# Performance work log

Measured on AMD Instinct MI355X. Metric: run time of the kernel, lower is better.

Reference implementation:

```python
import jax, jax.numpy as jnp
import numpy as np

S, B, I, H, L = 512, 64, 512, 512, 2
EPS = 1e-5


def setup_inputs() -> dict:
    key = jax.random.key(0)
    ks = jax.random.split(key, 8)
    gain = float(np.sqrt(1.0 / H))
    u = lambda k, shp: jax.random.uniform(k, shp, jnp.float32, -gain, gain)
    return {
        "inputs": jax.random.normal(ks[0], (S, B, I), jnp.float32),
        "h0": jnp.zeros((L, B, H), jnp.float32),
        "c0": jnp.zeros((L, B, H), jnp.float32),
        "wx0": u(ks[1], (I, 4 * H)),
        "wx1": u(ks[2], (H, 4 * H)),
        "wh0": u(ks[3], (H, 4 * H)),
        "wh1": u(ks[4], (H, 4 * H)),
        "bias": u(ks[5], (L, 4 * H)),
        "ln_gamma": jnp.ones((L, 4, H), jnp.float32),
        "ln_beta": jnp.zeros((L, 4, H), jnp.float32),
    }


def _layer(x, h, c, wx, wh, b, gamma, beta):
    # Precompute the input projection as one big GEMM: [S,B,4H]
    xg = jnp.einsum('sbi,ig->sbg', x, wx) + b

    def cell(carry, xg_t):
        h, c = carry
        gate = xg_t + h @ wh                      # [B, 4H]
        g = gate.reshape(B, 4, H)
        mu = jnp.mean(g, axis=-1, keepdims=True)
        var = jnp.var(g, axis=-1, keepdims=True)
        g = (g - mu) * jax.lax.rsqrt(var + EPS) * gamma + beta
        i, f, o, u = g[:, 0], g[:, 1], g[:, 2], g[:, 3]
        c = jax.nn.sigmoid(f) * c + jax.nn.sigmoid(i) * jnp.tanh(u)
        h = jax.nn.sigmoid(o) * jnp.tanh(c)
        return (h, c), h

    (h, c), ys = jax.lax.scan(cell, (h, c), xg)
    return ys, h, c


def reference(inputs, h0, c0, wx0, wx1, wh0, wh1, bias, ln_gamma, ln_beta):
    x = inputs
    wxs, whs = [wx0, wx1], [wh0, wh1]
    hs, cs = [], []
    for l in range(L):
        x, h, c = _layer(x, h0[l], c0[l], wxs[l], whs[l], bias[l], ln_gamma[l], ln_beta[l])
        hs.append(h)
        cs.append(c)
    return x, jnp.stack(hs, 0), jnp.stack(cs, 0)
```

## Files before the change

kernel.cpp:

```cpp
#include <hip/hip_runtime.h>


typedef float f32x4 __attribute__((ext_vector_type(4)));

__device__ __forceinline__ float sigm(float x) { return 1.f / (1.f + __expf(-x)); }
__device__ __forceinline__ float tanh_f(float x) { return 2.f / (1.f + __expf(-2.f * x)) - 1.f; }

__global__ void init_k(const float* __restrict__ h0, const float* __restrict__ c0,
                       float* __restrict__ h_T, float* __restrict__ c_ws) {
  const int nthr = gridDim.x * 256;
  for (int i = blockIdx.x * 256 + threadIdx.x; i < 2 * 64 * 512; i += nthr) {
    int l = i >> 15, rem = i & 32767, b = rem >> 9, hc = rem & 511;
    h_T[(l * 512 + hc) * 64 + b] = h0[i];
    c_ws[i] = c0[i];
  }
}

__global__ __launch_bounds__(256)
void gemm_step(const float* __restrict__ inputs,
               const float* __restrict__ wx0, const float* __restrict__ wx1,
               const float* __restrict__ wh0, const float* __restrict__ wh1,
               const float* __restrict__ bias,
               const float* __restrict__ h_T, const float* __restrict__ y0_T,
               float* __restrict__ gates_ws, int tau)
{
  extern __shared__ float lds[];
  float* W_lds = lds;
  float* A_lds = lds + 16384;
  float* part  = lds + 33792;

  const int tid = threadIdx.x;
  const int wg = blockIdx.x;
  const int layer = wg >> 7;
  const int w = wg & 127;
  if (layer == 0 ? (tau >= 512) : (tau < 1)) return;
  const int t = layer ? (tau - 1) : tau;

  const int wavet = tid >> 6, lane = tid & 63;
  const int rq = lane & 15;
  const int gq = lane >> 4;
  const int srow = tid >> 2, sg = tid & 3;

  const float* Wx = layer ? wx1 : wx0;
  const float* Wh = layer ? wh1 : wh0;

  for (int i = 0; i < 16; ++i) {
    int e = tid + i * 256;
    int k = e >> 2, g = e & 3;
    const float* src = (k < 512) ? (Wx + (size_t)k * 2048)
                                 : (Wh + (size_t)(k - 512) * 2048);
    *(f32x4*)&W_lds[k * 16 + g * 4] = *(const f32x4*)(src + g * 512 + 4 * w);
  }
  __syncthreads();

  f32x4 biasr = *(const f32x4*)(bias + layer * 2048 + sg * 512 + 4 * w);
  f32x4 acc[4];
#pragma unroll
  for (int r = 0; r < 4; ++r) acc[r] = (f32x4){0.f, 0.f, 0.f, 0.f};

  {
    const float* hT = h_T + layer * 32768;
    const int k0 = wavet * 128;
#pragma unroll 8
    for (int kk = 0; kk < 128; ++kk) {
      int k = k0 + kk;
      f32x4 av = *(const f32x4*)&hT[k * 64 + 4 * rq];
      f32x4 wv = *(const f32x4*)&W_lds[(512 + k) * 16 + gq * 4];
      acc[0] += av[0] * wv;
      acc[1] += av[1] * wv;
      acc[2] += av[2] * wv;
      acc[3] += av[3] * wv;
    }
  }

  if (layer == 1) {
    const int k0 = wavet * 128;
#pragma unroll 8
    for (int kk = 0; kk < 128; ++kk) {
      int k = k0 + kk;
      f32x4 av = *(const f32x4*)&y0_T[k * 64 + 4 * rq];
      f32x4 wv = *(const f32x4*)&W_lds[k * 16 + gq * 4];
      acc[0] += av[0] * wv;
      acc[1] += av[1] * wv;
      acc[2] += av[2] * wv;
      acc[3] += av[3] * wv;
    }
  } else {
    const float* xsrc = inputs + (size_t)t * 32768;
    const int strow = rq + 16 * wavet;
    f32x4 st[8];
    auto LOADC = [&](int koff) {
      const float* s = xsrc + strow * 512 + koff;
#pragma unroll
      for (int i = 0; i < 8; ++i)
        st[i] = *(const f32x4*)(s + 4 * (gq + 4 * i));
    };
    auto WRITEC = [&](int b) {
      float* dst = A_lds + b * 8704;
#pragma unroll
      for (int i = 0; i < 8; ++i) {
        int kq = gq + 4 * i;
#pragma unroll
        for (int j = 0; j < 4; ++j)
          dst[(4 * kq + j) * 68 + strow] = st[i][j];
      }
    };
    LOADC(0);
    WRITEC(0);
    __syncthreads();
#pragma unroll 1
    for (int i = 0; i < 4; ++i) {
      if (i < 3) LOADC((i + 1) * 128);
      const float* Ab = A_lds + (i & 1) * 8704;
      const int kg = i * 128 + wavet * 32;
#pragma unroll 8
      for (int kk = 0; kk < 32; ++kk) {
        int k = wavet * 32 + kk;
        f32x4 av = *(const f32x4*)&Ab[k * 68 + 4 * rq];
        f32x4 wv = *(const f32x4*)&W_lds[(kg + kk) * 16 + gq * 4];
        acc[0] += av[0] * wv;
        acc[1] += av[1] * wv;
        acc[2] += av[2] * wv;
        acc[3] += av[3] * wv;
      }
      if (i < 3) WRITEC((i + 1) & 1);
      __syncthreads();
    }
  }

#pragma unroll
  for (int r = 0; r < 4; ++r)
#pragma unroll
    for (int cc = 0; cc < 4; ++cc)
      part[(wavet * 64 + 4 * rq + r) * 17 + gq * 4 + cc] = acc[r][cc];
  __syncthreads();
  {
    f32x4 pre;
#pragma unroll
    for (int cc = 0; cc < 4; ++cc) {
      float v = biasr[cc];
      v += part[(0 * 64 + srow) * 17 + sg * 4 + cc];
      v += part[(1 * 64 + srow) * 17 + sg * 4 + cc];
      v += part[(2 * 64 + srow) * 17 + sg * 4 + cc];
      v += part[(3 * 64 + srow) * 17 + sg * 4 + cc];
      pre[cc] = v;
    }
    *(f32x4*)&gates_ws[((size_t)layer * 64 + srow) * 2048 + sg * 512 + 4 * w] = pre;
  }
}

__global__ __launch_bounds__(256)
void cell_step(const float* __restrict__ gates_ws,
               const float* __restrict__ gamma_, const float* __restrict__ beta_,
               float* __restrict__ c_ws, float* __restrict__ h_T,
               float* __restrict__ y0_T, float* __restrict__ out, int tau)
{
  __shared__ float sred[512];
  __shared__ float minv[8];
  __shared__ float gnorm[2048];

  const int tid = threadIdx.x;
  const int wgid = blockIdx.x;
  const int l = wgid >> 6, b = wgid & 63;
  if (l == 0 ? (tau >= 512) : (tau < 1)) return;
  const int t = l ? (tau - 1) : tau;

  const float* grow = gates_ws + ((size_t)l * 64 + b) * 2048;
  const int c0i = tid * 8;
  float acc[8];
#pragma unroll
  for (int j = 0; j < 8; ++j) acc[j] = grow[c0i + j];

  {
    float s = 0.f, ss = 0.f;
#pragma unroll
    for (int j = 0; j < 8; ++j) { s += acc[j]; ss += acc[j] * acc[j]; }
    sred[tid * 2] = s; sred[tid * 2 + 1] = ss;
  }
  __syncthreads();
  if (tid < 4) {
    float S = 0.f, SS = 0.f;
    for (int u = 0; u < 64; ++u) {
      S += sred[(tid * 64 + u) * 2];
      SS += sred[(tid * 64 + u) * 2 + 1];
    }
    float mu = S * (1.f / 512.f);
    float var = SS * (1.f / 512.f) - mu * mu;
    minv[tid * 2] = mu;
    minv[tid * 2 + 1] = rsqrtf(fmaxf(var, 0.f) + 1e-5f);
  }
  __syncthreads();
  {
    int g = tid >> 6;
    float mu = minv[g * 2], inv = minv[g * 2 + 1];
#pragma unroll
    for (int j = 0; j < 8; ++j) {
      int c = c0i + j;
      gnorm[c] = (acc[j] - mu) * inv * gamma_[l * 2048 + c] + beta_[l * 2048 + c];
    }
  }
  __syncthreads();

#pragma unroll
  for (int v = 0; v < 2; ++v) {
    int hc = tid * 2 + v;
    float ig = sigm(gnorm[hc]);
    float fg = sigm(gnorm[512 + hc]);
    float og = sigm(gnorm[1024 + hc]);
    float ug = tanh_f(gnorm[1536 + hc]);
    float cs = fg * c_ws[l * 32768 + b * 512 + hc] + ig * ug;
    float hv = og * tanh_f(cs);
    c_ws[l * 32768 + b * 512 + hc] = cs;
    h_T[(l * 512 + hc) * 64 + b] = hv;
    if (l == 0) y0_T[hc * 64 + b] = hv;
    else        out[(size_t)t * 32768 + b * 512 + hc] = hv;
    if (t == 511) {
      out[16777216 + l * 32768 + b * 512 + hc] = hv;
      out[16842752 + l * 32768 + b * 512 + hc] = cs;
    }
  }
}

extern "C" void kernel_launch(void* const* d_in, const int* in_sizes, int n_in,
                              void* d_out, int out_size, void* d_ws, size_t ws_size,
                              hipStream_t stream) {
  const float* inputs = (const float*)d_in[0];
  const float* h0 = (const float*)d_in[1];
  const float* c0 = (const float*)d_in[2];
  const float* wx0 = (const float*)d_in[3];
  const float* wx1 = (const float*)d_in[4];
  const float* wh0 = (const float*)d_in[5];
  const float* wh1 = (const float*)d_in[6];
  const float* bias = (const float*)d_in[7];
  const float* gamma_ = (const float*)d_in[8];
  const float* beta_ = (const float*)d_in[9];
  float* out = (float*)d_out;

  char* ws = (char*)d_ws;
  float* gates_ws = (float*)ws;
  float* h_T = (float*)(ws + 1048576);
  float* y0_T = (float*)(ws + 1310720);
  float* c_ws = (float*)(ws + 1441792);

  const int smem_bytes = 38144 * 4;
  hipFuncSetAttribute((const void*)gemm_step,
                      hipFuncAttributeMaxDynamicSharedMemorySize, smem_bytes);

  hipLaunchKernelGGL(init_k, dim3(256), dim3(256), 0, stream, h0, c0, h_T, c_ws);

  for (int tau = 0; tau <= 512; ++tau) {
    hipLaunchKernelGGL(gemm_step, dim3(256), dim3(256), smem_bytes, stream,
                       inputs, wx0, wx1, wh0, wh1, bias, h_T, y0_T, gates_ws, tau);
    hipLaunchKernelGGL(cell_step, dim3(128), dim3(256), 0, stream,
                       gates_ws, gamma_, beta_, c_ws, h_T, y0_T, out, tau);
  }
}
```

Baseline: 20.71 ms.

## Pre-transpose next timestep's input in cell kernel, drop LDS transpose in GEMM

Layer-0 GEMM blocks no longer load the input slice and transpose it through LDS with double buffering. Instead, the cell_step kernel transposes the next timestep's input into a ping-pong x_T buffer, and init_k transposes step 0. The GEMM then reads x_T directly from global memory, the same way it reads h_T. This removes the per-block redundant transpose, several barriers and about 68KB of LDS, which may allow more blocks per CU. The cost is uncoalesced strided reads in cell_step and a new cross-kernel dependency on the ping-pong buffer.

```diff
diff --git a/kernel.cpp b/kernel.cpp
--- a/kernel.cpp
+++ b/kernel.cpp
@@ -6,18 +6,24 @@
 __device__ __forceinline__ float sigm(float x) { return 1.f / (1.f + __expf(-x)); }
 __device__ __forceinline__ float tanh_f(float x) { return 2.f / (1.f + __expf(-2.f * x)) - 1.f; }
 
-__global__ void init_k(const float* __restrict__ h0, const float* __restrict__ c0,
-                       float* __restrict__ h_T, float* __restrict__ c_ws) {
+__global__ void init_k(const float* __restrict__ inputs,
+                       const float* __restrict__ h0, const float* __restrict__ c0,
+                       float* __restrict__ h_T, float* __restrict__ c_ws,
+                       float* __restrict__ x_T) {
   const int nthr = gridDim.x * 256;
   for (int i = blockIdx.x * 256 + threadIdx.x; i < 2 * 64 * 512; i += nthr) {
     int l = i >> 15, rem = i & 32767, b = rem >> 9, hc = rem & 511;
     h_T[(l * 512 + hc) * 64 + b] = h0[i];
     c_ws[i] = c0[i];
   }
+  for (int i = blockIdx.x * 256 + threadIdx.x; i < 512 * 64; i += nthr) {
+    int k = i >> 6, b = i & 63;
+    x_T[k * 64 + b] = inputs[b * 512 + k];
+  }
 }
 
 __global__ __launch_bounds__(256)
-void gemm_step(const float* __restrict__ inputs,
+void gemm_step(const float* __restrict__ x_T,
                const float* __restrict__ wx0, const float* __restrict__ wx1,
                const float* __restrict__ wh0, const float* __restrict__ wh1,
                const float* __restrict__ bias,
@@ -26,15 +32,13 @@
 {
   extern __shared__ float lds[];
   float* W_lds = lds;
-  float* A_lds = lds + 16384;
-  float* part  = lds + 33792;
+  float* part  = lds + 16384;
 
   const int tid = threadIdx.x;
   const int wg = blockIdx.x;
   const int layer = wg >> 7;
   const int w = wg & 127;
   if (layer == 0 ? (tau >= 512) : (tau < 1)) return;
-  const int t = layer ? (tau - 1) : tau;
 
   const int wavet = tid >> 6, lane = tid & 63;
   const int rq = lane & 15;
@@ -58,75 +62,22 @@
 #pragma unroll
   for (int r = 0; r < 4; ++r) acc[r] = (f32x4){0.f, 0.f, 0.f, 0.f};
 
-  {
-    const float* hT = h_T + layer * 32768;
+  auto GEMMT = [&](const float* T, int wbase) {
     const int k0 = wavet * 128;
 #pragma unroll 8
     for (int kk = 0; kk < 128; ++kk) {
       int k = k0 + kk;
-      f32x4 av = *(const f32x4*)&hT[k * 64 + 4 * rq];
-      f32x4 wv = *(const f32x4*)&W_lds[(512 + k) * 16 + gq * 4];
+      f32x4 av = *(const f32x4*)&T[k * 64 + 4 * rq];
+      f32x4 wv = *(const f32x4*)&W_lds[(wbase + k) * 16 + gq * 4];
       acc[0] += av[0] * wv;
       acc[1] += av[1] * wv;
       acc[2] += av[2] * wv;
       acc[3] += av[3] * wv;
     }
-  }
-
-  if (layer == 1) {
-    const int k0 = wavet * 128;
-#pragma unroll 8
-    for (int kk = 0; kk < 128; ++kk) {
-      int k = k0 + kk;
-      f32x4 av = *(const f32x4*)&y0_T[k * 64 + 4 * rq];
-      f32x4 wv = *(const f32x4*)&W_lds[k * 16 + gq * 4];
-      acc[0] += av[0] * wv;
-      acc[1] += av[1] * wv;
-      acc[2] += av[2] * wv;
-      acc[3] += av[3] * wv;
-    }
-  } else {
-    const float* xsrc = inputs + (size_t)t * 32768;
-    const int strow = rq + 16 * wavet;
-    f32x4 st[8];
-    auto LOADC = [&](int koff) {
-      const float* s = xsrc + strow * 512 + koff;
-#pragma unroll
-      for (int i = 0; i < 8; ++i)
-        st[i] = *(const f32x4*)(s + 4 * (gq + 4 * i));
-    };
-    auto WRITEC = [&](int b) {
-      float* dst = A_lds + b * 8704;
-#pragma unroll
-      for (int i = 0; i < 8; ++i) {
-        int kq = gq + 4 * i;
-#pragma unroll
-        for (int j = 0; j < 4; ++j)
-          dst[(4 * kq + j) * 68 + strow] = st[i][j];
-      }
-    };
-    LOADC(0);
-    WRITEC(0);
-    __syncthreads();
-#pragma unroll 1
-    for (int i = 0; i < 4; ++i) {
-      if (i < 3) LOADC((i + 1) * 128);
-      const float* Ab = A_lds + (i & 1) * 8704;
-      const int kg = i * 128 + wavet * 32;
-#pragma unroll 8
-      for (int kk = 0; kk < 32; ++kk) {
-        int k = wavet * 32 + kk;
-        f32x4 av = *(const f32x4*)&Ab[k * 68 + 4 * rq];
-        f32x4 wv = *(const f32x4*)&W_lds[(kg + kk) * 16 + gq * 4];
-        acc[0] += av[0] * wv;
-        acc[1] += av[1] * wv;
-        acc[2] += av[2] * wv;
-        acc[3] += av[3] * wv;
-      }
-      if (i < 3) WRITEC((i + 1) & 1);
-      __syncthreads();
-    }
-  }
+  };
+
+  GEMMT(h_T + layer * 32768, 512);
+  GEMMT(layer ? y0_T : (x_T + (size_t)(tau & 1) * 32768), 0);
 
 #pragma unroll
   for (int r = 0; r < 4; ++r)
@@ -152,8 +103,10 @@
 __global__ __launch_bounds__(256)
 void cell_step(const float* __restrict__ gates_ws,
                const float* __restrict__ gamma_, const float* __restrict__ beta_,
+               const float* __restrict__ inputs,
                float* __restrict__ c_ws, float* __restrict__ h_T,
-               float* __restrict__ y0_T, float* __restrict__ out, int tau)
+               float* __restrict__ y0_T, float* __restrict__ x_T,
+               float* __restrict__ out, int tau)
 {
   __shared__ float sred[512];
   __shared__ float minv[8];
@@ -170,6 +123,15 @@
   float acc[8];
 #pragma unroll
   for (int j = 0; j < 8; ++j) acc[j] = grow[c0i + j];
+
+  if (l == 0 && tau < 511) {
+    const float* xn = inputs + (size_t)(tau + 1) * 32768;
+    float* xd = x_T + (size_t)((tau + 1) & 1) * 32768;
+    int e0 = b * 512 + tid * 2;
+    int k = e0 >> 6, b2 = e0 & 63;
+    xd[k * 64 + b2] = xn[b2 * 512 + k];
+    xd[k * 64 + b2 + 1] = xn[(b2 + 1) * 512 + k];
+  }
 
   {
     float s = 0.f, ss = 0.f;
@@ -241,17 +203,19 @@
   float* h_T = (float*)(ws + 1048576);
   float* y0_T = (float*)(ws + 1310720);
   float* c_ws = (float*)(ws + 1441792);
-
-  const int smem_bytes = 38144 * 4;
+  float* x_T = (float*)(ws + 1703936);
+
+  const int smem_bytes = 20736 * 4;
   hipFuncSetAttribute((const void*)gemm_step,
                       hipFuncAttributeMaxDynamicSharedMemorySize, smem_bytes);
 
-  hipLaunchKernelGGL(init_k, dim3(256), dim3(256), 0, stream, h0, c0, h_T, c_ws);
+  hipLaunchKernelGGL(init_k, dim3(256), dim3(256), 0, stream,
+                     inputs, h0, c0, h_T, c_ws, x_T);
 
   for (int tau = 0; tau <= 512; ++tau) {
     hipLaunchKernelGGL(gemm_step, dim3(256), dim3(256), smem_bytes, stream,
-                       inputs, wx0, wx1, wh0, wh1, bias, h_T, y0_T, gates_ws, tau);
+                       x_T, wx0, wx1, wh0, wh1, bias, h_T, y0_T, gates_ws, tau);
     hipLaunchKernelGGL(cell_step, dim3(128), dim3(256), 0, stream,
-                       gates_ws, gamma_, beta_, c_ws, h_T, y0_T, out, tau);
-  }
-}
+                       gates_ws, gamma_, beta_, inputs, c_ws, h_T, y0_T, x_T, out, tau);
+  }
+}
```

New measurement: 43.81 ms. 2.12x slower.
